# Kernel tuning notes

Hardware: AMD Instinct MI355X
Metric: run time of the kernel (lower is better)

## Reference

```python
import jax, jax.numpy as jnp
import numpy as np

# ---- Clifford algebra G(3,0,1) (projective GA) blade tables, built once in numpy ----
_BLADES = [(), (0,), (1,), (2,), (3,), (0, 1), (0, 2), (0, 3), (1, 2), (1, 3), (2, 3), (0, 1, 2), (0, 1, 3), (0, 2, 3), (1, 2, 3), (0, 1, 2, 3)]
_IDX = {b: i for i, b in enumerate(_BLADES)}
_METRIC = [0.0, 1.0, 1.0, 1.0]  # e0^2 = 0 (degenerate), e1..e3 square to +1

def _blade_mul(a, b):
    arr = list(a) + list(b)
    sign = 1.0
    swapped = True
    while swapped:  # bubble sort, tracking permutation sign
        swapped = False
        for j in range(len(arr) - 1):
            if arr[j] > arr[j + 1]:
                arr[j], arr[j + 1] = arr[j + 1], arr[j]
                sign = -sign
                swapped = True
    res = []
    j = 0
    while j < len(arr):
        if j + 1 < len(arr) and arr[j] == arr[j + 1]:
            sign *= _METRIC[arr[j]]
            j += 2
        else:
            res.append(arr[j])
            j += 1
    return sign, tuple(res)

_GP = np.zeros((16, 16, 16), np.float32)    # geometric product Cayley table
_WEDGE = np.zeros((16, 16, 16), np.float32)  # outer (wedge) product table
for _i, _a in enumerate(_BLADES):
    for _j, _b in enumerate(_BLADES):
        _s, _r = _blade_mul(_a, _b)
        if _s != 0.0:
            _GP[_i, _j, _IDX[_r]] = _s
        if set(_a).isdisjoint(_b):
            _WEDGE[_i, _j, _IDX[_r]] = _s

# dual = right complement: e_a ^ dual(e_a) = e0123 (metric-free, valid in degenerate PGA)
_D = np.zeros((16, 16), np.float32)
for _i, _a in enumerate(_BLADES):
    _comp = tuple(sorted(set(range(4)) - set(_a)))
    _D[_i, _IDX[_comp]] = _WEDGE[_i, _IDX[_comp], 15]
_UND = np.linalg.inv(_D).astype(np.float32)
# join(x, y) = undual(dual(x) ^ dual(y)) as a single 16^3 trilinear table
_JOIN = np.einsum('ia,jb,abc,ck->ijk', _D, _D, _WEDGE, _UND).astype(np.float32)
_GRADES = np.array([len(b) for b in _BLADES])

GP_T = jnp.asarray(_GP)
JOIN_T = jnp.asarray(_JOIN)
GRADES = jnp.asarray(_GRADES)


def _equilin(x, w):
    # Equivariant linear layer: one channel-mixing matrix per grade.
    # x: [B, N, Cin, 16], w: [5, Cout, Cin] -> [B, N, Cout, 16]
    wk = w[GRADES]  # [16, Cout, Cin]
    return jnp.einsum('bnik,koi->bnok', x, wk)


def setup_inputs() -> dict:
    key = jax.random.key(0)
    ks = jax.random.split(key, 7)
    B, N, Cin, Cout = 32, 1024, 64, 64
    H = Cout // 2
    s_in = 1.0 / np.sqrt(Cin)
    s_out = 1.0 / np.sqrt(Cout)
    return {
        'x': jax.random.normal(ks[0], (B, N, Cin, 16), jnp.float32),
        'ref': jax.random.normal(ks[1], (B, N, 16), jnp.float32),
        'w_prodX': jax.random.normal(ks[2], (5, H, Cin), jnp.float32) * s_in,
        'w_prodY': jax.random.normal(ks[3], (5, H, Cin), jnp.float32) * s_in,
        'w_joinX': jax.random.normal(ks[4], (5, H, Cin), jnp.float32) * s_in,
        'w_joinY': jax.random.normal(ks[5], (5, H, Cin), jnp.float32) * s_in,
        'w_final': jax.random.normal(ks[6], (5, Cout, Cout), jnp.float32) * s_out,
    }


def reference(x, ref, w_prodX, w_prodY, w_joinX, w_joinY, w_final):
    # geometric product branch
    px = _equilin(x, w_prodX)
    py = _equilin(x, w_prodY)
    prod = jnp.einsum('bnci,bncj,ijk->bnck', px, py, GP_T)
    # equivariant join branch, scaled by reference pseudoscalar coefficient (GATr)
    jx = _equilin(x, w_joinX)
    jy = _equilin(x, w_joinY)
    join = jnp.einsum('bnci,bncj,ijk->bnck', jx, jy, JOIN_T)
    join = join * ref[..., 15][..., None, None]
    feats = jnp.concatenate([prod, join], axis=-2)  # [B, N, Cout, 16]
    return _equilin(feats, w_final)
```

## Files before the change

### kernel.cpp

```cpp
#include <hip/hip_runtime.h>
#include <stdint.h>


#define BN 32768

typedef __attribute__((ext_vector_type(2))) _Float16 h2;
typedef __attribute__((ext_vector_type(8))) _Float16 h8;
typedef __attribute__((ext_vector_type(4))) float f32x4;

#define MFMA_F16 __builtin_amdgcn_mfma_f32_16x16x32_f16

__device__ __forceinline__ h2 pk(float a, float b) {
  return (h2)__builtin_amdgcn_cvt_pkrtz(a, b);
}

constexpr int IDX2MASK[16] = {0,1,2,4,8,3,5,9,6,10,12,7,11,13,14,15};
constexpr int MASK2IDX[16] = {0,1,2,5,3,6,8,11,4,7,9,12,10,13,14,15};

struct MulRes { float s; int idx; };

constexpr MulRes blade_mul(int ia, int ib) {
  int arr[8] = {0,0,0,0,0,0,0,0}; int n = 0;
  for (int e = 0; e < 4; ++e) if ((IDX2MASK[ia] >> e) & 1) arr[n++] = e;
  for (int e = 0; e < 4; ++e) if ((IDX2MASK[ib] >> e) & 1) arr[n++] = e;
  float sign = 1.0f;
  bool sw = true;
  while (sw) {
    sw = false;
    for (int j = 0; j + 1 < n; ++j)
      if (arr[j] > arr[j+1]) { int t = arr[j]; arr[j] = arr[j+1]; arr[j+1] = t; sign = -sign; sw = true; }
  }
  int mask = 0; int j = 0;
  while (j < n) {
    if (j + 1 < n && arr[j] == arr[j+1]) { if (arr[j] == 0) sign = 0.0f; j += 2; }
    else { mask |= 1 << arr[j]; ++j; }
  }
  return MulRes{sign, MASK2IDX[mask]};
}

constexpr float dual_sign(int i) {
  return blade_mul(i, MASK2IDX[15 ^ IDX2MASK[i]]).s;
}

struct Tab { float s[16][16]; int k[16][16]; };

constexpr Tab make_gp() {
  Tab t{};
  for (int i = 0; i < 16; ++i)
    for (int j = 0; j < 16; ++j) { MulRes r = blade_mul(i, j); t.s[i][j] = r.s; t.k[i][j] = r.idx; }
  return t;
}

constexpr Tab make_join() {
  Tab t{};
  for (int i = 0; i < 16; ++i)
    for (int j = 0; j < 16; ++j) {
      int ma = 15 ^ IDX2MASK[i], mb = 15 ^ IDX2MASK[j];
      if (ma & mb) { t.s[i][j] = 0.0f; t.k[i][j] = 0; continue; }
      int ia = MASK2IDX[ma], ib = MASK2IDX[mb];
      MulRes w = blade_mul(ia, ib);
      int kk = MASK2IDX[15 ^ IDX2MASK[w.idx]];
      t.s[i][j] = dual_sign(i) * dual_sign(j) * w.s * dual_sign(kk);
      t.k[i][j] = kk;
    }
  return t;
}

constexpr Tab GPT = make_gp();
constexpr Tab JNT = make_join();
constexpr int GRADE[16] = {0,1,1,1,1,2,2,2,2,2,2,3,3,3,3,4};
constexpr int GSTART[6] = {0,1,5,11,15,16};

struct KTab { int cnt[16]; int ti[16][16]; int tj[16][16]; float ts[16][16]; };
constexpr KTab make_ktab(const Tab& t) {
  KTab b{};
  for (int i = 0; i < 16; ++i)
    for (int j = 0; j < 16; ++j) {
      float s = t.s[i][j];
      if (s != 0.f) { int k = t.k[i][j]; int m = b.cnt[k]; b.cnt[k] = m + 1;
                      b.ti[k][m] = i; b.tj[k][m] = j; b.ts[k][m] = s; }
    }
  return b;
}
constexpr KTab GPK = make_ktab(GPT);
constexpr KTab JNK = make_ktab(JNT);

__device__ __forceinline__ int lds_sh(int k, int tok, int s) {
  return k * 1024 + tok * 64 + (s ^ (((k + tok) & 7) << 3));
}

__device__ __align__(16) short g_wpre_h[4 * 5 * 32 * 64];
__device__ __align__(16) short g_wfin_h[5 * 64 * 64];

__global__ void cast_weights(const float* __restrict__ wpx, const float* __restrict__ wpy,
                             const float* __restrict__ wjx, const float* __restrict__ wjy,
                             const float* __restrict__ wf) {
  int idx = blockIdx.x * 256 + threadIdx.x;
  if (idx < 40960) {
    int which = idx / 10240, r = idx % 10240;
    const float* src = (which == 0) ? wpx : (which == 1) ? wpy : (which == 2) ? wjx : wjy;
    _Float16 h = (_Float16)src[r];
    g_wpre_h[idx] = __builtin_bit_cast(short, h);
  } else if (idx < 40960 + 20480) {
    int r = idx - 40960;
    _Float16 h = (_Float16)wf[r];
    g_wfin_h[r] = __builtin_bit_cast(short, h);
  }
}

__global__ __launch_bounds__(256, 4) void gbl_kernel(
    const float* __restrict__ x,
    const float* __restrict__ ref,
    float* __restrict__ out)
{
  __shared__ __align__(16) short ldsb[16 * 1024];

  const int tid  = threadIdx.x;
  const int w    = tid >> 6;
  const int lane = tid & 63;
  const int n    = lane & 15;
  const int q    = lane >> 4;
  const int t0   = blockIdx.x * 16;
  const int br   = w >> 1, nt = w & 1;

  float refv[4];
  if (br == 1) {
    #pragma unroll
    for (int r = 0; r < 4; ++r) refv[r] = ref[(size_t)(t0 + 4 * q + r) * 16 + 15];
  }

  {
    const int k  = tid & 15;
    const int tt = tid >> 4;
    const float* xr = x + (size_t)(t0 + tt) * 1024 + k;
    #pragma unroll
    for (int ib = 0; ib < 8; ++ib) {
      float v[8];
      #pragma unroll
      for (int j = 0; j < 8; ++j) v[j] = xr[(ib * 8 + j) * 16];
      uint32_t u0 = __builtin_bit_cast(uint32_t, pk(v[0], v[1]));
      uint32_t u1 = __builtin_bit_cast(uint32_t, pk(v[2], v[3]));
      uint32_t u2 = __builtin_bit_cast(uint32_t, pk(v[4], v[5]));
      uint32_t u3 = __builtin_bit_cast(uint32_t, pk(v[6], v[7]));
      uint4 pv = make_uint4(u0, u1, u2, u3);
      *(uint4*)&ldsb[lds_sh(k, tt, ib * 8)] = pv;
    }
  }
  __syncthreads();

  h2 pxh[16][2], pyh[16][2];
  {
    #pragma unroll
    for (int g = 0; g < 5; ++g) {
      const short* bx = &g_wpre_h[(((br * 2 + 0) * 5 + g) * 32 + nt * 16 + n) * 64 + q * 8];
      const short* by = &g_wpre_h[(((br * 2 + 1) * 5 + g) * 32 + nt * 16 + n) * 64 + q * 8];
      h8 Bx0 = *(const h8*)(bx), Bx1 = *(const h8*)(bx + 32);
      h8 By0 = *(const h8*)(by), By1 = *(const h8*)(by + 32);
      #pragma unroll
      for (int kb = GSTART[g]; kb < GSTART[g + 1]; ++kb) {
        h8 a0 = *(const h8*)&ldsb[lds_sh(kb, n, q * 8)];
        h8 a1 = *(const h8*)&ldsb[lds_sh(kb, n, 32 + q * 8)];
        f32x4 ax = {0.f, 0.f, 0.f, 0.f};
        ax = MFMA_F16(a0, Bx0, ax, 0, 0, 0);
        ax = MFMA_F16(a1, Bx1, ax, 0, 0, 0);
        pxh[kb][0] = pk(ax[0], ax[1]);
        pxh[kb][1] = pk(ax[2], ax[3]);
        f32x4 ay = {0.f, 0.f, 0.f, 0.f};
        ay = MFMA_F16(a0, By0, ay, 0, 0, 0);
        ay = MFMA_F16(a1, By1, ay, 0, 0, 0);
        pyh[kb][0] = pk(ay[0], ay[1]);
        pyh[kb][1] = pk(ay[2], ay[3]);
      }
    }
  }
  __syncthreads();

  {
    h2 rv0, rv1;
    if (br == 1) { rv0 = pk(refv[0], refv[1]); rv1 = pk(refv[2], refv[3]); }
    const int cg = w * 16 + n;
    #pragma unroll
    for (int k = 0; k < 16; ++k) {
      h2 a0 = (_Float16)0.0f, a1 = (_Float16)0.0f;
      if (br == 0) {
        #pragma unroll
        for (int m = 0; m < 16; ++m) {
          if (m < GPK.cnt[k]) {
            const int i = GPK.ti[k][m], j = GPK.tj[k][m];
            if (GPK.ts[k][m] < 0.f) { a0 -= pxh[i][0] * pyh[j][0]; a1 -= pxh[i][1] * pyh[j][1]; }
            else                    { a0 += pxh[i][0] * pyh[j][0]; a1 += pxh[i][1] * pyh[j][1]; }
          }
        }
      } else {
        #pragma unroll
        for (int m = 0; m < 16; ++m) {
          if (m < JNK.cnt[k]) {
            const int i = JNK.ti[k][m], j = JNK.tj[k][m];
            if (JNK.ts[k][m] < 0.f) { a0 -= pxh[i][0] * pyh[j][0]; a1 -= pxh[i][1] * pyh[j][1]; }
            else                    { a0 += pxh[i][0] * pyh[j][0]; a1 += pxh[i][1] * pyh[j][1]; }
          }
        }
        a0 *= rv0; a1 *= rv1;
      }
      uint32_t u0 = __builtin_bit_cast(uint32_t, a0);
      uint32_t u1 = __builtin_bit_cast(uint32_t, a1);
      ldsb[lds_sh(k, 4 * q + 0, cg)] = (short)(u0 & 0xffffu);
      ldsb[lds_sh(k, 4 * q + 1, cg)] = (short)(u0 >> 16);
      ldsb[lds_sh(k, 4 * q + 2, cg)] = (short)(u1 & 0xffffu);
      ldsb[lds_sh(k, 4 * q + 3, cg)] = (short)(u1 >> 16);
    }
  }
  __syncthreads();

  {
    const int o = w * 16 + n;
    f32x4 D[16];
    h8 BF0, BF1;
    #pragma unroll
    for (int kb = 0; kb < 16; ++kb) {
      if (kb == 0 || kb == 1 || kb == 5 || kb == 11 || kb == 15) {
        const short* bf = &g_wfin_h[(GRADE[kb] * 64 + o) * 64 + q * 8];
        BF0 = *(const h8*)(bf);
        BF1 = *(const h8*)(bf + 32);
      }
      h8 a0 = *(const h8*)&ldsb[lds_sh(kb, n, q * 8)];
      h8 a1 = *(const h8*)&ldsb[lds_sh(kb, n, 32 + q * 8)];
      f32x4 acc = {0.f, 0.f, 0.f, 0.f};
      acc = MFMA_F16(a0, BF0, acc, 0, 0, 0);
      acc = MFMA_F16(a1, BF1, acc, 0, 0, 0);
      D[kb] = acc;
    }

    #pragma unroll
    for (int r = 0; r < 4; ++r) {
      const int t = t0 + 4 * q + r;
      float4* op = (float4*)(out + (size_t)t * 1024 + o * 16);
      op[0] = make_float4(D[0][r],  D[1][r],  D[2][r],  D[3][r]);
      op[1] = make_float4(D[4][r],  D[5][r],  D[6][r],  D[7][r]);
      op[2] = make_float4(D[8][r],  D[9][r],  D[10][r], D[11][r]);
      op[3] = make_float4(D[12][r], D[13][r], D[14][r], D[15][r]);
    }
  }
}

extern "C" void kernel_launch(void* const* d_in, const int* in_sizes, int n_in,
                              void* d_out, int out_size, void* d_ws, size_t ws_size,
                              hipStream_t stream) {
  const float* x   = (const float*)d_in[0];
  const float* ref = (const float*)d_in[1];
  const float* wpx = (const float*)d_in[2];
  const float* wpy = (const float*)d_in[3];
  const float* wjx = (const float*)d_in[4];
  const float* wjy = (const float*)d_in[5];
  const float* wfi = (const float*)d_in[6];

  cast_weights<<<240, 256, 0, stream>>>(wpx, wpy, wjx, wjy, wfi);
  gbl_kernel<<<BN / 16, 256, 0, stream>>>(x, ref, (float*)d_out);
}
```

Before: 290.4 us.

## Process two token tiles per block with register prefetch of next x tile

Each block now handles two 16-token tiles. The next tile's x and ref values are prefetched into registers during the product stage, then written to LDS after the output stage, hiding global load latency. The x load is also switched to float4-vectorized reads, and outputs use nontemporal stores. In exchange the kernel uses more registers (launch bounds lowered to 3 waves per EU), launches half as many blocks, and adds an extra barrier per iteration.

After: 395.2 us. +36.1%, slower.

```diff
diff --git a/kernel.cpp b/kernel.cpp
--- a/kernel.cpp
+++ b/kernel.cpp
@@ -3,6 +3,8 @@
 
 
 #define BN 32768
+#define NT 2
+#define GRID (BN / 16 / NT)
 
 typedef __attribute__((ext_vector_type(2))) _Float16 h2;
 typedef __attribute__((ext_vector_type(8))) _Float16 h8;
@@ -108,7 +110,25 @@
   }
 }
 
-__global__ __launch_bounds__(256, 4) void gbl_kernel(
+__device__ __forceinline__ void stage_write(short* ldsb, int tok, int kq, int iq,
+                                            const f32x4* pf) {
+  #pragma unroll
+  for (int jk = 0; jk < 4; ++jk) {
+    const int k = kq * 4 + jk;
+    uint32_t c0 = __builtin_bit_cast(uint32_t, pk(pf[0][jk],  pf[1][jk]));
+    uint32_t c1 = __builtin_bit_cast(uint32_t, pk(pf[2][jk],  pf[3][jk]));
+    uint32_t c2 = __builtin_bit_cast(uint32_t, pk(pf[4][jk],  pf[5][jk]));
+    uint32_t c3 = __builtin_bit_cast(uint32_t, pk(pf[6][jk],  pf[7][jk]));
+    uint32_t c4 = __builtin_bit_cast(uint32_t, pk(pf[8][jk],  pf[9][jk]));
+    uint32_t c5 = __builtin_bit_cast(uint32_t, pk(pf[10][jk], pf[11][jk]));
+    uint32_t c6 = __builtin_bit_cast(uint32_t, pk(pf[12][jk], pf[13][jk]));
+    uint32_t c7 = __builtin_bit_cast(uint32_t, pk(pf[14][jk], pf[15][jk]));
+    *(uint4*)&ldsb[lds_sh(k, tok, iq * 16)]     = make_uint4(c0, c1, c2, c3);
+    *(uint4*)&ldsb[lds_sh(k, tok, iq * 16 + 8)] = make_uint4(c4, c5, c6, c7);
+  }
+}
+
+__global__ __launch_bounds__(256, 3) void gbl_kernel(
     const float* __restrict__ x,
     const float* __restrict__ ref,
     float* __restrict__ out)
@@ -120,40 +140,37 @@
   const int lane = tid & 63;
   const int n    = lane & 15;
   const int q    = lane >> 4;
-  const int t0   = blockIdx.x * 16;
-  const int br   = w >> 1, nt = w & 1;
-
-  float refv[4];
-  if (br == 1) {
+  const int br   = w >> 1, nth = w & 1;
+
+  const int stok = tid >> 4;
+  const int skq  = (tid >> 2) & 3;
+  const int siq  = tid & 3;
+
+  const int tile0 = blockIdx.x * NT;
+
+  f32x4 pf[16];
+  float refc[4], refn[4];
+
+  {
+    const float* base = x + (size_t)(tile0 * 16 + stok) * 1024 + (siq * 16) * 16 + skq * 4;
     #pragma unroll
-    for (int r = 0; r < 4; ++r) refv[r] = ref[(size_t)(t0 + 4 * q + r) * 16 + 15];
-  }
-
-  {
-    const int k  = tid & 15;
-    const int tt = tid >> 4;
-    const float* xr = x + (size_t)(t0 + tt) * 1024 + k;
-    #pragma unroll
-    for (int ib = 0; ib < 8; ++ib) {
-      float v[8];
-      #pragma unroll
-      for (int j = 0; j < 8; ++j) v[j] = xr[(ib * 8 + j) * 16];
-      uint32_t u0 = __builtin_bit_cast(uint32_t, pk(v[0], v[1]));
-      uint32_t u1 = __builtin_bit_cast(uint32_t, pk(v[2], v[3]));
-      uint32_t u2 = __builtin_bit_cast(uint32_t, pk(v[4], v[5]));
-      uint32_t u3 = __builtin_bit_cast(uint32_t, pk(v[6], v[7]));
-      uint4 pv = make_uint4(u0, u1, u2, u3);
-      *(uint4*)&ldsb[lds_sh(k, tt, ib * 8)] = pv;
-    }
-  }
-  __syncthreads();
-
-  h2 pxh[16][2], pyh[16][2];
-  {
+    for (int ii = 0; ii < 16; ++ii) pf[ii] = *(const f32x4*)(base + ii * 16);
+    if (br == 1) {
+      #pragma unroll
+      for (int r = 0; r < 4; ++r) refc[r] = ref[(size_t)(tile0 * 16 + 4 * q + r) * 16 + 15];
+    }
+  }
+  stage_write(ldsb, stok, skq, siq, pf);
+
+  for (int it = 0; it < NT; ++it) {
+    const int t0 = (tile0 + it) * 16;
+    __syncthreads();
+
+    h2 pxh[16][2], pyh[16][2];
     #pragma unroll
     for (int g = 0; g < 5; ++g) {
-      const short* bx = &g_wpre_h[(((br * 2 + 0) * 5 + g) * 32 + nt * 16 + n) * 64 + q * 8];
-      const short* by = &g_wpre_h[(((br * 2 + 1) * 5 + g) * 32 + nt * 16 + n) * 64 + q * 8];
+      const short* bx = &g_wpre_h[(((br * 2 + 0) * 5 + g) * 32 + nth * 16 + n) * 64 + q * 8];
+      const short* by = &g_wpre_h[(((br * 2 + 1) * 5 + g) * 32 + nth * 16 + n) * 64 + q * 8];
       h8 Bx0 = *(const h8*)(bx), Bx1 = *(const h8*)(bx + 32);
       h8 By0 = *(const h8*)(by), By1 = *(const h8*)(by + 32);
       #pragma unroll
@@ -172,73 +189,97 @@
         pyh[kb][1] = pk(ay[2], ay[3]);
       }
     }
-  }
-  __syncthreads();
-
-  {
-    h2 rv0, rv1;
-    if (br == 1) { rv0 = pk(refv[0], refv[1]); rv1 = pk(refv[2], refv[3]); }
-    const int cg = w * 16 + n;
-    #pragma unroll
-    for (int k = 0; k < 16; ++k) {
-      h2 a0 = (_Float16)0.0f, a1 = (_Float16)0.0f;
-      if (br == 0) {
+    __syncthreads();
+
+    if (it + 1 < NT) {
+      const float* base = x + (size_t)((tile0 + it + 1) * 16 + stok) * 1024
+                            + (siq * 16) * 16 + skq * 4;
+      #pragma unroll
+      for (int ii = 0; ii < 16; ++ii) pf[ii] = *(const f32x4*)(base + ii * 16);
+      if (br == 1) {
         #pragma unroll
-        for (int m = 0; m < 16; ++m) {
-          if (m < GPK.cnt[k]) {
-            const int i = GPK.ti[k][m], j = GPK.tj[k][m];
-            if (GPK.ts[k][m] < 0.f) { a0 -= pxh[i][0] * pyh[j][0]; a1 -= pxh[i][1] * pyh[j][1]; }
-            else                    { a0 += pxh[i][0] * pyh[j][0]; a1 += pxh[i][1] * pyh[j][1]; }
+        for (int r = 0; r < 4; ++r)
+          refn[r] = ref[(size_t)((tile0 + it + 1) * 16 + 4 * q + r) * 16 + 15];
+      }
+    }
+
+    {
+      h2 rv0, rv1;
+      if (br == 1) { rv0 = pk(refc[0], refc[1]); rv1 = pk(refc[2], refc[3]); }
+      const int cg = w * 16 + n;
+      #pragma unroll
+      for (int k = 0; k < 16; ++k) {
+        h2 a0 = (_Float16)0.0f, a1 = (_Float16)0.0f;
+        if (br == 0) {
+          #pragma unroll
+          for (int m = 0; m < 16; ++m) {
+            if (m < GPK.cnt[k]) {
+              const int i = GPK.ti[k][m], j = GPK.tj[k][m];
+              if (GPK.ts[k][m] < 0.f) { a0 -= pxh[i][0] * pyh[j][0]; a1 -= pxh[i][1] * pyh[j][1]; }
+              else                    { a0 += pxh[i][0] * pyh[j][0]; a1 += pxh[i][1] * pyh[j][1]; }
+            }
           }
+        } else {
+          #pragma unroll
+          for (int m = 0; m < 16; ++m) {
+            if (m < JNK.cnt[k]) {
+              const int i = JNK.ti[k][m], j = JNK.tj[k][m];
+              if (JNK.ts[k][m] < 0.f) { a0 -= pxh[i][0] * pyh[j][0]; a1 -= pxh[i][1] * pyh[j][1]; }
+              else                    { a0 += pxh[i][0] * pyh[j][0]; a1 += pxh[i][1] * pyh[j][1]; }
+            }
+          }
+          a0 *= rv0; a1 *= rv1;
         }
-      } else {
+        uint32_t u0 = __builtin_bit_cast(uint32_t, a0);
+        uint32_t u1 = __builtin_bit_cast(uint32_t, a1);
+        ldsb[lds_sh(k, 4 * q + 0, cg)] = (short)(u0 & 0xffffu);
+        ldsb[lds_sh(k, 4 * q + 1, cg)] = (short)(u0 >> 16);
+        ldsb[lds_sh(k, 4 * q + 2, cg)] = (short)(u1 & 0xffffu);
+        ldsb[lds_sh(k, 4 * q + 3, cg)] = (short)(u1 >> 16);
+      }
+    }
+    __syncthreads();
+
+    {
+      const int o = w * 16 + n;
+      f32x4 D[16];
+      h8 BF0, BF1;
+      #pragma unroll
+      for (int kb = 0; kb < 16; ++kb) {
+        if (kb == 0 || kb == 1 || kb == 5 || kb == 11 || kb == 15) {
+          const short* bf = &g_wfin_h[(GRADE[kb] * 64 + o) * 64 + q * 8];
+          BF0 = *(const h8*)(bf);
+          BF1 = *(const h8*)(bf + 32);
+        }
+        h8 a0 = *(const h8*)&ldsb[lds_sh(kb, n, q * 8)];
+        h8 a1 = *(const h8*)&ldsb[lds_sh(kb, n, 32 + q * 8)];
+        f32x4 acc = {0.f, 0.f, 0.f, 0.f};
+        acc = MFMA_F16(a0, BF0, acc, 0, 0, 0);
+        acc = MFMA_F16(a1, BF1, acc, 0, 0, 0);
+        D[kb] = acc;
+      }
+      #pragma unroll
+      for (int r = 0; r < 4; ++r) {
+        const int t = t0 + 4 * q + r;
+        f32x4* op = (f32x4*)(out + (size_t)t * 1024 + o * 16);
+        f32x4 s0 = {D[0][r],  D[1][r],  D[2][r],  D[3][r]};
+        f32x4 s1 = {D[4][r],  D[5][r],  D[6][r],  D[7][r]};
+        f32x4 s2 = {D[8][r],  D[9][r],  D[10][r], D[11][r]};
+        f32x4 s3 = {D[12][r], D[13][r], D[14][r], D[15][r]};
+        __builtin_nontemporal_store(s0, op + 0);
+        __builtin_nontemporal_store(s1, op + 1);
+        __builtin_nontemporal_store(s2, op + 2);
+        __builtin_nontemporal_store(s3, op + 3);
+      }
+    }
+
+    if (it + 1 < NT) {
+      __syncthreads();
+      stage_write(ldsb, stok, skq, siq, pf);
+      if (br == 1) {
         #pragma unroll
-        for (int m = 0; m < 16; ++m) {
-          if (m < JNK.cnt[k]) {
-            const int i = JNK.ti[k][m], j = JNK.tj[k][m];
-            if (JNK.ts[k][m] < 0.f) { a0 -= pxh[i][0] * pyh[j][0]; a1 -= pxh[i][1] * pyh[j][1]; }
-            else                    { a0 += pxh[i][0] * pyh[j][0]; a1 += pxh[i][1] * pyh[j][1]; }
-          }
-        }
-        a0 *= rv0; a1 *= rv1;
-      }
-      uint32_t u0 = __builtin_bit_cast(uint32_t, a0);
-      uint32_t u1 = __builtin_bit_cast(uint32_t, a1);
-      ldsb[lds_sh(k, 4 * q + 0, cg)] = (short)(u0 & 0xffffu);
-      ldsb[lds_sh(k, 4 * q + 1, cg)] = (short)(u0 >> 16);
-      ldsb[lds_sh(k, 4 * q + 2, cg)] = (short)(u1 & 0xffffu);
-      ldsb[lds_sh(k, 4 * q + 3, cg)] = (short)(u1 >> 16);
-    }
-  }
-  __syncthreads();
-
-  {
-    const int o = w * 16 + n;
-    f32x4 D[16];
-    h8 BF0, BF1;
-    #pragma unroll
-    for (int kb = 0; kb < 16; ++kb) {
-      if (kb == 0 || kb == 1 || kb == 5 || kb == 11 || kb == 15) {
-        const short* bf = &g_wfin_h[(GRADE[kb] * 64 + o) * 64 + q * 8];
-        BF0 = *(const h8*)(bf);
-        BF1 = *(const h8*)(bf + 32);
-      }
-      h8 a0 = *(const h8*)&ldsb[lds_sh(kb, n, q * 8)];
-      h8 a1 = *(const h8*)&ldsb[lds_sh(kb, n, 32 + q * 8)];
-      f32x4 acc = {0.f, 0.f, 0.f, 0.f};
-      acc = MFMA_F16(a0, BF0, acc, 0, 0, 0);
-      acc = MFMA_F16(a1, BF1, acc, 0, 0, 0);
-      D[kb] = acc;
-    }
-
-    #pragma unroll
-    for (int r = 0; r < 4; ++r) {
-      const int t = t0 + 4 * q + r;
-      float4* op = (float4*)(out + (size_t)t * 1024 + o * 16);
-      op[0] = make_float4(D[0][r],  D[1][r],  D[2][r],  D[3][r]);
-      op[1] = make_float4(D[4][r],  D[5][r],  D[6][r],  D[7][r]);
-      op[2] = make_float4(D[8][r],  D[9][r],  D[10][r], D[11][r]);
-      op[3] = make_float4(D[12][r], D[13][r], D[14][r], D[15][r]);
+        for (int r = 0; r < 4; ++r) refc[r] = refn[r];
+      }
     }
   }
 }
@@ -255,5 +296,5 @@
   const float* wfi = (const float*)d_in[6];
 
   cast_weights<<<240, 256, 0, stream>>>(wpx, wpy, wjx, wjy, wfi);
-  gbl_kernel<<<BN / 16, 256, 0, stream>>>(x, ref, (float*)d_out);
-}
+  gbl_kernel<<<GRID, 256, 0, stream>>>(x, ref, (float*)d_out);
+}
```
